# Kernel tuning notes

Measured on AMD Instinct MI355X. Metric: run time of the kernel, lower is better.

## Reference

```python
import jax, jax.numpy as jnp
import numpy as np

N = 12288
E = 393216
IN_DIM = 128
HID = 64
QK = 32
K_HOPS = 2


def setup_inputs() -> dict:
    key = jax.random.key(0)
    ks = jax.random.split(key, 12)
    s = lambda k, shp, fan: jax.random.normal(k, shp, jnp.float32) / np.sqrt(fan)
    return {
        "x_train": jax.random.normal(ks[0], (N, IN_DIM), jnp.float32),
        "x_ori": jax.random.normal(ks[1], (N, IN_DIM), jnp.float32),
        "edge_index": jax.random.randint(ks[2], (2, E), 0, N, jnp.int64),
        "mask": jnp.zeros((N,), jnp.bool_),
        "W1": s(ks[3], (IN_DIM, HID), IN_DIM), "b1": jnp.zeros((HID,), jnp.float32),
        "W2": s(ks[4], (HID, HID), HID),      "b2": jnp.zeros((HID,), jnp.float32),
        "Wq": s(ks[5], (HID, QK), HID),       "bq": jnp.zeros((QK,), jnp.float32),
        "Wk": s(ks[6], (HID, QK), HID),       "bk": jnp.zeros((QK,), jnp.float32),
        "Wv": s(ks[7], (HID, HID), HID),      "bv": jnp.zeros((HID,), jnp.float32),
        "Wdx": s(ks[8], (HID, IN_DIM), HID),  "bdx": jnp.zeros((IN_DIM,), jnp.float32),
    }


def reference(x_train, x_ori, edge_index, mask,
              W1, b1, W2, b2, Wq, bq, Wk, bk, Wv, bv, Wdx, bdx):
    n = x_train.shape[0]
    row, col = edge_index[0], edge_index[1]

    # shared MLP: linear -> relu -> linear2 -> relu
    enc = lambda x: jax.nn.relu(jax.nn.relu(x @ W1 + b1) @ W2 + b2)
    h_ori = enc(x_ori)      # [N, HID]
    h_train = enc(x_train)  # [N, HID]

    # degree of source nodes, D^{-1/2}
    deg = jax.ops.segment_sum(jnp.ones_like(row, jnp.float32), row, num_segments=n)
    d_invsqrt = jnp.clip(deg, 1.0, None) ** -0.5  # [N]
    d_invsqrt = d_invsqrt[:, None]

    def lap(x):
        h = x * d_invsqrt
        out = jax.ops.segment_sum(h[row], col, num_segments=n)
        return x - out * d_invsqrt

    a_feat = 2.0 * h_train - lap(h_train)  # low-pass: 2I - L_sym
    stack = [a_feat]
    x = h_train
    for _ in range(K_HOPS):  # dropout inert in eval mode
        x = lap(x)
        stack.append(x)
    L = jnp.stack(stack, axis=1)  # [N, K+1, HID]

    # attention with global mean-pooled query over h_ori[~mask]
    w = (~mask).astype(jnp.float32)
    q_nodes = h_ori @ Wq + bq                              # [N, QK]
    q_global = (q_nodes * w[:, None]).sum(0) / jnp.clip(w.sum(), 1.0, None)  # [QK]
    keys = L @ Wk + bk   # [N, K+1, QK]
    vals = L @ Wv + bv   # [N, K+1, HID]
    scale = 1.0 / np.sqrt(HID)  # scale uses D = keys feature dim BEFORE projection
    scores = jnp.einsum('q,nkq->nk', q_global, keys) * scale
    A = jax.nn.softmax(scores, axis=-1)          # [N, K+1]
    z = jnp.einsum('nk,nkd->nd', A, vals)        # [N, HID]

    x_hat = z @ Wdx + bdx   # [N, IN_DIM]
    adj_hat = z @ z.T       # [N, N]
    return x_hat, adj_hat
```

## Files before the change

### kernel.cpp

```cpp
#include <hip/hip_runtime.h>
#include <hip/hip_bf16.h>

constexpr int N_  = 12288;
constexpr int E_  = 393216;
constexpr int IND = 128;
constexpr int HID = 64;
constexpr int QKD = 32;

typedef __attribute__((ext_vector_type(4))) float f4raw;
typedef __attribute__((ext_vector_type(8))) __bf16 bf16x8;
typedef __attribute__((ext_vector_type(4))) __bf16 bf16x4;
typedef __attribute__((ext_vector_type(16))) float f32x16;

__device__ inline bf16x8 lds_read_bf8(const char* base, int row, int k) {
  int off = (row * 128 + k * 2) ^ ((row & 7) << 4);
  uint4 u = *(const uint4*)(base + off);
  union { uint4 u; bf16x8 v; } c; c.u = u; return c.v;
}
__device__ inline void lds_write_bf(char* base, int row, int col, __bf16 v) {
  int off = (row * 128 + col * 2) ^ ((row & 7) << 4);
  *(__bf16*)(base + off) = v;
}

__global__ __launch_bounds__(256) void prep_hist_kernel(
    const float* __restrict__ xo, const float* __restrict__ xt,
    const int* __restrict__ row, const int* __restrict__ col,
    const float* __restrict__ W1, const float* __restrict__ W2,
    const float* __restrict__ Wv, const float* __restrict__ Wdx,
    __bf16* __restrict__ xb, __bf16* __restrict__ W1T, __bf16* __restrict__ W2T,
    __bf16* __restrict__ WvT, __bf16* __restrict__ WdxT,
    int* degRow, int* cntCol) {
  int b = blockIdx.x, tid = threadIdx.x;
  if (b < 1536) {
    int e = b * 256 + tid;
    atomicAdd(&degRow[row[e]], 1);
    atomicAdd(&cntCol[col[e]], 1);
  } else if (b < 3072) {
    size_t base = (size_t)(b - 1536) * 2048 + (size_t)tid * 8;
    const size_t half = (size_t)N_ * IND;
    const float* src = (base < half) ? (xo + base) : (xt + (base - half));
    f4raw v0 = *(const f4raw*)(src);
    f4raw v1 = *(const f4raw*)(src + 4);
    bf16x8 o;
    o[0] = (__bf16)v0.x; o[1] = (__bf16)v0.y; o[2] = (__bf16)v0.z; o[3] = (__bf16)v0.w;
    o[4] = (__bf16)v1.x; o[5] = (__bf16)v1.y; o[6] = (__bf16)v1.z; o[7] = (__bf16)v1.w;
    *(bf16x8*)(xb + base) = o;
  } else if (b == 3072) {
    for (int e = tid; e < IND * HID; e += 256) {
      int c = e >> 7, k = e & 127;
      W1T[e] = (__bf16)W1[k * HID + c];
    }
  } else if (b == 3073) {
    for (int e = tid; e < HID * HID; e += 256) {
      int c = e >> 6, k = e & 63;
      W2T[e] = (__bf16)W2[k * HID + c];
    }
  } else if (b == 3074) {
    for (int e = tid; e < HID * HID; e += 256) {
      int c = e >> 6, k = e & 63;
      WvT[e] = (__bf16)Wv[k * HID + c];
    }
  } else {
    for (int e = tid; e < HID * IND; e += 256) {
      int c = e >> 6, k = e & 63;
      WdxT[e] = (__bf16)Wdx[k * IND + c];
    }
  }
}

__global__ __launch_bounds__(1024) void scan_kernel(const int* __restrict__ cnt,
                                                    const int* __restrict__ deg,
                                                    int* __restrict__ off,
                                                    int* __restrict__ cursor,
                                                    float* __restrict__ dinv) {
  __shared__ int sd[1024];
  int tid = threadIdx.x;
  int base = tid * 12;
  int local[12];
  int s = 0;
#pragma unroll
  for (int i = 0; i < 12; ++i) { local[i] = cnt[base + i]; s += local[i]; }
  sd[tid] = s;
  __syncthreads();
  for (int o = 1; o < 1024; o <<= 1) {
    int v = (tid >= o) ? sd[tid - o] : 0;
    __syncthreads();
    sd[tid] += v;
    __syncthreads();
  }
  int run = sd[tid] - s;
#pragma unroll
  for (int i = 0; i < 12; ++i) {
    off[base + i] = run;
    cursor[base + i] = run;
    run += local[i];
  }
  if (tid == 1023) off[N_] = run;
#pragma unroll
  for (int i = 0; i < 12; ++i) {
    int ii = base + i;
    dinv[ii] = rsqrtf((float)max(deg[ii], 1));
  }
}

__global__ __launch_bounds__(256) void scatter_enc_kernel(
    const int* __restrict__ row, const int* __restrict__ col,
    int* cursor, int* __restrict__ csrRow,
    const __bf16* __restrict__ xb,
    const __bf16* __restrict__ W1T, const float* __restrict__ b1,
    const __bf16* __restrict__ W2T, const float* __restrict__ b2,
    const float* __restrict__ dinv, const unsigned char* __restrict__ mask,
    float* __restrict__ h_tr, float* __restrict__ xd, float* __restrict__ gsum) {
  __shared__ __align__(16) char h1s[2][32 * 128];
  __shared__ float wls[64];
  int b = blockIdx.x, tid = threadIdx.x;
  if (b < 1536) {
    int e = b * 256 + tid;
    int c = col[e];
    int p = atomicAdd(&cursor[c], 1);
    csrRow[p] = row[e];
    return;
  }
  int bb = b - 1536;
  bool ori = bb < 192;
  int row0 = (ori ? bb : bb - 192) * 64;
  const __bf16* xrow = xb + (ori ? (size_t)0 : (size_t)N_ * IND) + (size_t)row0 * IND;
  if (tid < 64) wls[tid] = ori ? (mask[row0 + tid] ? 0.f : 1.f) : dinv[row0 + tid];
  int wave = tid >> 6, lane = tid & 63;
  int p = wave >> 1, w2 = wave & 1;
  int lr = lane & 31, hi = lane >> 5;
  int colc = w2 * 32 + lr;
  f32x16 acc = (f32x16)(0.f);
  const __bf16* wcol = W1T + (size_t)colc * IND + hi * 8;
  const __bf16* arow = xrow + (size_t)(p * 32 + lr) * IND + hi * 8;
#pragma unroll
  for (int kk = 0; kk < 8; ++kk) {
    bf16x8 a = *(const bf16x8*)(arow + kk * 16);
    bf16x8 bq = *(const bf16x8*)(wcol + kk * 16);
    acc = __builtin_amdgcn_mfma_f32_32x32x16_bf16(a, bq, acc, 0, 0, 0);
  }
  float b1l = b1[colc];
#pragma unroll
  for (int reg = 0; reg < 16; ++reg) {
    int rr = (reg & 3) + 8 * (reg >> 2) + 4 * hi;
    float v = fmaxf(acc[reg] + b1l, 0.f);
    lds_write_bf(h1s[p], rr, colc, (__bf16)v);
  }
  __syncthreads();
  f32x16 acc2 = (f32x16)(0.f);
  const __bf16* wcol2 = W2T + (size_t)colc * HID + hi * 8;
#pragma unroll
  for (int kk = 0; kk < 4; ++kk) {
    bf16x8 a = lds_read_bf8(h1s[p], lr, kk * 16 + hi * 8);
    bf16x8 bq = *(const bf16x8*)(wcol2 + kk * 16);
    acc2 = __builtin_amdgcn_mfma_f32_32x32x16_bf16(a, bq, acc2, 0, 0, 0);
  }
  float b2l = b2[colc];
  if (ori) {
    float part = 0.f;
#pragma unroll
    for (int reg = 0; reg < 16; ++reg) {
      int rr = (reg & 3) + 8 * (reg >> 2) + 4 * hi;
      float v = fmaxf(acc2[reg] + b2l, 0.f);
      part = fmaf(wls[p * 32 + rr], v, part);
    }
    atomicAdd(&gsum[colc], part);
    if (tid == 0) {
      float wl = 0.f;
      for (int r = 0; r < 64; ++r) wl += wls[r];
      atomicAdd(&gsum[64], wl);
    }
  } else {
#pragma unroll
    for (int reg = 0; reg < 16; ++reg) {
      int rr = (reg & 3) + 8 * (reg >> 2) + 4 * hi;
      float v = fmaxf(acc2[reg] + b2l, 0.f);
      int gr = row0 + p * 32 + rr;
      h_tr[(size_t)gr * HID + colc] = v;
      xd[(size_t)gr * HID + colc] = v * wls[p * 32 + rr];
    }
  }
}

__global__ __launch_bounds__(256) void lap1_kernel(
    const float* __restrict__ xd, const float* __restrict__ dinv,
    const int* __restrict__ off, const int* __restrict__ csrRow,
    float* __restrict__ lap1d) {
  int lane = threadIdx.x & 63, wv = threadIdx.x >> 6;
  int g = lane >> 4, t = lane & 15;
  int c = blockIdx.x * 16 + wv * 4 + g;
  int s0 = off[c], s1 = off[c + 1];
  f4raw a0 = (f4raw)(0.f), a1 = (f4raw)(0.f);
  int i = s0;
  for (; i + 1 < s1; i += 2) {
    int r0 = csrRow[i], r1 = csrRow[i + 1];
    a0 += *(const f4raw*)(xd + (size_t)r0 * HID + t * 4);
    a1 += *(const f4raw*)(xd + (size_t)r1 * HID + t * 4);
  }
  if (i < s1) {
    int r0 = csrRow[i];
    a0 += *(const f4raw*)(xd + (size_t)r0 * HID + t * 4);
  }
  float d = dinv[c];
  size_t idx = (size_t)c * HID + t * 4;
  *(f4raw*)(lap1d + idx) = *(const f4raw*)(xd + idx) - (a0 + a1) * (d * d);
}

__global__ __launch_bounds__(256) void lap2_kernel(
    const float* __restrict__ lap1d, const float* __restrict__ dinv,
    const int* __restrict__ off, const int* __restrict__ csrRow,
    float* __restrict__ lap2) {
  int lane = threadIdx.x & 63, wv = threadIdx.x >> 6;
  int g = lane >> 4, t = lane & 15;
  int c = blockIdx.x * 16 + wv * 4 + g;
  int s0 = off[c], s1 = off[c + 1];
  f4raw a0 = (f4raw)(0.f), a1 = (f4raw)(0.f);
  int i = s0;
  for (; i + 1 < s1; i += 2) {
    int r0 = csrRow[i], r1 = csrRow[i + 1];
    a0 += *(const f4raw*)(lap1d + (size_t)r0 * HID + t * 4);
    a1 += *(const f4raw*)(lap1d + (size_t)r1 * HID + t * 4);
  }
  if (i < s1) {
    int r0 = csrRow[i];
    a0 += *(const f4raw*)(lap1d + (size_t)r0 * HID + t * 4);
  }
  float d = dinv[c];
  float rd = 1.0f / d;
  size_t idx = (size_t)c * HID + t * 4;
  *(f4raw*)(lap2 + idx) = *(const f4raw*)(lap1d + idx) * rd - (a0 + a1) * d;
}

__global__ __launch_bounds__(128) void attnz_xhat_kernel(
    const float* __restrict__ h, const float* __restrict__ lap1d,
    const float* __restrict__ lap2, const float* __restrict__ dinv,
    const float* __restrict__ gsum,
    const float* __restrict__ Wq, const float* __restrict__ bq,
    const float* __restrict__ Wk, const float* __restrict__ bk,
    const __bf16* __restrict__ WvT, const float* __restrict__ bv,
    const __bf16* __restrict__ WdxT, const float* __restrict__ bdx,
    float* __restrict__ xhat, __bf16* __restrict__ zb) {
  __shared__ __align__(16) char zps[32 * 128];
  __shared__ __align__(16) char zsl[32 * 128];
  __shared__ float qg[QKD];
  __shared__ float kqs[72];
  int tid = threadIdx.x;
  float wsum = gsum[64];
  if (tid < QKD) {
    float inv = 1.0f / fmaxf(wsum, 1.0f);
    float a = bq[tid] * wsum;
    for (int d0 = 0; d0 < HID; ++d0) a = fmaf(gsum[d0], Wq[d0 * QKD + tid], a);
    qg[tid] = a * inv;
  }
  __syncthreads();
  if (tid < 64) {
    float a = 0.f;
    for (int q = 0; q < QKD; ++q) a = fmaf(Wk[tid * QKD + q], qg[q], a);
    kqs[tid] = a * 0.125f;
  } else if (tid == 64) {
    float sb = 0.f;
    for (int q = 0; q < QKD; ++q) sb = fmaf(bk[q], qg[q], sb);
    kqs[64] = sb * 0.125f;
  }
  __syncthreads();
  int wave = tid >> 6, lane = tid & 63;
  int g = lane >> 4, t = lane & 15;
  int row0 = blockIdx.x * 32;
  f4raw kq4 = *(const f4raw*)(&kqs[t * 4]);
  float sbias = kqs[64];
#pragma unroll
  for (int it = 0; it < 4; ++it) {
    int r = wave * 16 + it * 4 + g;
    int c = row0 + r;
    size_t idx = (size_t)c * HID + t * 4;
    float d = dinv[c];
    float rd = 1.0f / d;
    f4raw hv = *(const f4raw*)(h + idx);
    f4raw v1 = *(const f4raw*)(lap1d + idx) * rd;
    f4raw v2 = *(const f4raw*)(lap2 + idx);
    f4raw av = 2.f * hv - v1;
    float s0 = av.x * kq4.x + av.y * kq4.y + av.z * kq4.z + av.w * kq4.w;
    float s1 = v1.x * kq4.x + v1.y * kq4.y + v1.z * kq4.z + v1.w * kq4.w;
    float s2 = v2.x * kq4.x + v2.y * kq4.y + v2.z * kq4.z + v2.w * kq4.w;
#pragma unroll
    for (int o = 1; o < 16; o <<= 1) {
      s0 += __shfl_xor(s0, o);
      s1 += __shfl_xor(s1, o);
      s2 += __shfl_xor(s2, o);
    }
    s0 += sbias; s1 += sbias; s2 += sbias;
    float m = fmaxf(s0, fmaxf(s1, s2));
    float e0 = __expf(s0 - m), e1 = __expf(s1 - m), e2 = __expf(s2 - m);
    float is = 1.f / (e0 + e1 + e2);
    f4raw zp = (e0 * av + e1 * v1 + e2 * v2) * is;
    bf16x4 z4;
    z4[0] = (__bf16)zp.x; z4[1] = (__bf16)zp.y; z4[2] = (__bf16)zp.z; z4[3] = (__bf16)zp.w;
    int off = (r * 128 + t * 8) ^ ((r & 7) << 4);
    *(bf16x4*)(zps + off) = z4;
  }
  __syncthreads();
  int lr = lane & 31, hi = lane >> 5;
  int col = wave * 32 + lr;
  f32x16 accz = (f32x16)(0.f);
  const __bf16* wv = WvT + (size_t)col * HID + hi * 8;
#pragma unroll
  for (int kk = 0; kk < 4; ++kk) {
    bf16x8 a = lds_read_bf8(zps, lr, kk * 16 + hi * 8);
    bf16x8 bq = *(const bf16x8*)(wv + kk * 16);
    accz = __builtin_amdgcn_mfma_f32_32x32x16_bf16(a, bq, accz, 0, 0, 0);
  }
  float bvl = bv[col];
#pragma unroll
  for (int reg = 0; reg < 16; ++reg) {
    int rr = (reg & 3) + 8 * (reg >> 2) + 4 * hi;
    __bf16 vb = (__bf16)(accz[reg] + bvl);
    zb[(size_t)(row0 + rr) * HID + col] = vb;
    lds_write_bf(zsl, rr, col, vb);
  }
  __syncthreads();
#pragma unroll
  for (int tt = 0; tt < 2; ++tt) {
    int c0 = wave * 32 + tt * 64 + lr;
    f32x16 acx = (f32x16)(0.f);
    const __bf16* wd = WdxT + (size_t)c0 * HID + hi * 8;
#pragma unroll
    for (int kk = 0; kk < 4; ++kk) {
      bf16x8 a = lds_read_bf8(zsl, lr, kk * 16 + hi * 8);
      bf16x8 bq = *(const bf16x8*)(wd + kk * 16);
      acx = __builtin_amdgcn_mfma_f32_32x32x16_bf16(a, bq, acx, 0, 0, 0);
    }
    float bdl = bdx[c0];
#pragma unroll
    for (int reg = 0; reg < 16; ++reg) {
      int rr = (reg & 3) + 8 * (reg >> 2) + 4 * hi;
      xhat[(size_t)(row0 + rr) * IND + c0] = acx[reg] + bdl;
    }
  }
}

__global__ __launch_bounds__(256) void adj_mfma_kernel(
    const __bf16* __restrict__ z, float* __restrict__ out) {
  int tid = threadIdx.x;
  int wave = tid >> 6, lane = tid & 63;
  int wr = wave >> 1, wc = wave & 1;
  int rb = blockIdx.y, cb = blockIdx.x;
  int lr = lane & 31, hi = lane >> 5;

  size_t arow0 = (size_t)(rb * 128 + wr * 64 + lr) * HID;
  size_t arow1 = arow0 + (size_t)32 * HID;
  size_t brow0 = (size_t)(cb * 128 + wc * 64 + lr) * HID;
  size_t brow1 = brow0 + (size_t)32 * HID;
  int kbase = hi * 8;

  f32x16 acc00 = (f32x16)(0.f), acc01 = (f32x16)(0.f);
  f32x16 acc10 = (f32x16)(0.f), acc11 = (f32x16)(0.f);

#pragma unroll
  for (int kk = 0; kk < 4; ++kk) {
    int k0 = kk * 16 + kbase;
    bf16x8 a0 = *(const bf16x8*)(z + arow0 + k0);
    bf16x8 a1 = *(const bf16x8*)(z + arow1 + k0);
    bf16x8 b0 = *(const bf16x8*)(z + brow0 + k0);
    bf16x8 b1 = *(const bf16x8*)(z + brow1 + k0);
    acc00 = __builtin_amdgcn_mfma_f32_32x32x16_bf16(a0, b0, acc00, 0, 0, 0);
    acc01 = __builtin_amdgcn_mfma_f32_32x32x16_bf16(a0, b1, acc01, 0, 0, 0);
    acc10 = __builtin_amdgcn_mfma_f32_32x32x16_bf16(a1, b0, acc10, 0, 0, 0);
    acc11 = __builtin_amdgcn_mfma_f32_32x32x16_bf16(a1, b1, acc11, 0, 0, 0);
  }

  int colb = cb * 128 + wc * 64 + lr;
  int rowb = rb * 128 + wr * 64 + 4 * hi;
#pragma unroll
  for (int reg = 0; reg < 16; ++reg) {
    int rr = (reg & 3) + 8 * (reg >> 2);
    size_t r0 = (size_t)(rowb + rr);
    __builtin_nontemporal_store(acc00[reg], out + r0 * N_ + colb);
    __builtin_nontemporal_store(acc01[reg], out + r0 * N_ + colb + 32);
    __builtin_nontemporal_store(acc10[reg], out + (r0 + 32) * N_ + colb);
    __builtin_nontemporal_store(acc11[reg], out + (r0 + 32) * N_ + colb + 32);
  }
}

extern "C" void kernel_launch(void* const* d_in, const int* in_sizes, int n_in,
                              void* d_out, int out_size, void* d_ws, size_t ws_size,
                              hipStream_t stream) {
  const float* x_train = (const float*)d_in[0];
  const float* x_ori   = (const float*)d_in[1];
  const int*   ei      = (const int*)d_in[2];
  const unsigned char* mask = (const unsigned char*)d_in[3];
  const float* W1  = (const float*)d_in[4];
  const float* b1  = (const float*)d_in[5];
  const float* W2  = (const float*)d_in[6];
  const float* b2  = (const float*)d_in[7];
  const float* Wq  = (const float*)d_in[8];
  const float* bq  = (const float*)d_in[9];
  const float* Wk  = (const float*)d_in[10];
  const float* bk  = (const float*)d_in[11];
  const float* Wv  = (const float*)d_in[12];
  const float* bv  = (const float*)d_in[13];
  const float* Wdx = (const float*)d_in[14];
  const float* bdx = (const float*)d_in[15];

  char* ws = (char*)d_ws;
  size_t o = 0;
  auto alloc = [&](size_t bytes) -> void* {
    void* p = ws + o;
    o += (bytes + 255) & ~(size_t)255;
    return p;
  };
  __bf16* xb    = (__bf16*)alloc((size_t)2 * N_ * IND * 2);
  __bf16* W1T   = (__bf16*)alloc((size_t)IND * HID * 2);
  __bf16* W2T   = (__bf16*)alloc((size_t)HID * HID * 2);
  __bf16* WvT   = (__bf16*)alloc((size_t)HID * HID * 2);
  __bf16* WdxT  = (__bf16*)alloc((size_t)HID * IND * 2);
  float* h_tr   = (float*)alloc((size_t)N_ * HID * 4);
  float* lap1d  = (float*)alloc((size_t)N_ * HID * 4);
  float* lap2   = (float*)alloc((size_t)N_ * HID * 4);
  float* xd     = (float*)alloc((size_t)N_ * HID * 4);
  __bf16* zb    = (__bf16*)alloc((size_t)N_ * HID * 2);
  float* dinv   = (float*)alloc((size_t)N_ * 4);
  int*   zero0  = (int*)alloc((size_t)(2 * N_ + 65) * 4);
  int*   degRow = zero0;
  int*   cntCol = zero0 + N_;
  float* gsum   = (float*)(zero0 + 2 * N_);
  int*   off    = (int*)alloc((size_t)(N_ + 1) * 4);
  int*   cursor = (int*)alloc((size_t)N_ * 4);
  int*   csrRow = (int*)alloc((size_t)E_ * 4);

  const int* row = ei;
  const int* col = ei + E_;

  (void)hipMemsetAsync(zero0, 0, (size_t)(2 * N_ + 65) * 4, stream);

  prep_hist_kernel<<<3076, 256, 0, stream>>>(x_ori, x_train, row, col,
                                             W1, W2, Wv, Wdx,
                                             xb, W1T, W2T, WvT, WdxT,
                                             degRow, cntCol);
  scan_kernel<<<1, 1024, 0, stream>>>(cntCol, degRow, off, cursor, dinv);
  scatter_enc_kernel<<<1920, 256, 0, stream>>>(row, col, cursor, csrRow,
                                               xb, W1T, b1, W2T, b2,
                                               dinv, mask, h_tr, xd, gsum);
  lap1_kernel<<<N_ / 16, 256, 0, stream>>>(xd, dinv, off, csrRow, lap1d);
  lap2_kernel<<<N_ / 16, 256, 0, stream>>>(lap1d, dinv, off, csrRow, lap2);

  float* outp = (float*)d_out;
  attnz_xhat_kernel<<<N_ / 32, 128, 0, stream>>>(h_tr, lap1d, lap2, dinv, gsum,
                                                 Wq, bq, Wk, bk, WvT, bv,
                                                 WdxT, bdx, outp, zb);
  adj_mfma_kernel<<<dim3(96, 96), 256, 0, stream>>>(zb, outp + (size_t)N_ * IND);
}
```

Before: 270.0 us.

## Replace prefix-scan CSR with fixed-capacity buckets and fuse lap2 into attention

```diff
diff --git a/kernel.cpp b/kernel.cpp
--- a/kernel.cpp
+++ b/kernel.cpp
@@ -6,6 +6,7 @@
 constexpr int IND = 128;
 constexpr int HID = 64;
 constexpr int QKD = 32;
+constexpr int CAP = 96;
 
 typedef __attribute__((ext_vector_type(4))) float f4raw;
 typedef __attribute__((ext_vector_type(8))) __bf16 bf16x8;
@@ -22,21 +23,33 @@
   *(__bf16*)(base + off) = v;
 }
 
-__global__ __launch_bounds__(256) void prep_hist_kernel(
+__global__ __launch_bounds__(256) void prep_graph_kernel(
     const float* __restrict__ xo, const float* __restrict__ xt,
     const int* __restrict__ row, const int* __restrict__ col,
     const float* __restrict__ W1, const float* __restrict__ W2,
     const float* __restrict__ Wv, const float* __restrict__ Wdx,
     __bf16* __restrict__ xb, __bf16* __restrict__ W1T, __bf16* __restrict__ W2T,
     __bf16* __restrict__ WvT, __bf16* __restrict__ WdxT,
-    int* degRow, int* cntCol) {
+    int* degRow, int* cntCol, int* __restrict__ csrRow) {
   int b = blockIdx.x, tid = threadIdx.x;
-  if (b < 1536) {
-    int e = b * 256 + tid;
-    atomicAdd(&degRow[row[e]], 1);
-    atomicAdd(&cntCol[col[e]], 1);
-  } else if (b < 3072) {
-    size_t base = (size_t)(b - 1536) * 2048 + (size_t)tid * 8;
+  if (b < 384) {
+    int e0 = (b * 256 + tid) * 4;
+    int4 r4 = *(const int4*)(row + e0);
+    atomicAdd(&degRow[r4.x], 1);
+    atomicAdd(&degRow[r4.y], 1);
+    atomicAdd(&degRow[r4.z], 1);
+    atomicAdd(&degRow[r4.w], 1);
+  } else if (b < 768) {
+    int e0 = ((b - 384) * 256 + tid) * 4;
+    int4 r4 = *(const int4*)(row + e0);
+    int4 c4 = *(const int4*)(col + e0);
+    int p;
+    p = atomicAdd(&cntCol[c4.x], 1); csrRow[c4.x * CAP + p] = r4.x;
+    p = atomicAdd(&cntCol[c4.y], 1); csrRow[c4.y * CAP + p] = r4.y;
+    p = atomicAdd(&cntCol[c4.z], 1); csrRow[c4.z * CAP + p] = r4.z;
+    p = atomicAdd(&cntCol[c4.w], 1); csrRow[c4.w * CAP + p] = r4.w;
+  } else if (b < 2304) {
+    size_t base = (size_t)(b - 768) * 2048 + (size_t)tid * 8;
     const size_t half = (size_t)N_ * IND;
     const float* src = (base < half) ? (xo + base) : (xt + (base - half));
     f4raw v0 = *(const f4raw*)(src);
@@ -45,17 +58,17 @@
     o[0] = (__bf16)v0.x; o[1] = (__bf16)v0.y; o[2] = (__bf16)v0.z; o[3] = (__bf16)v0.w;
     o[4] = (__bf16)v1.x; o[5] = (__bf16)v1.y; o[6] = (__bf16)v1.z; o[7] = (__bf16)v1.w;
     *(bf16x8*)(xb + base) = o;
-  } else if (b == 3072) {
+  } else if (b == 2304) {
     for (int e = tid; e < IND * HID; e += 256) {
       int c = e >> 7, k = e & 127;
       W1T[e] = (__bf16)W1[k * HID + c];
     }
-  } else if (b == 3073) {
+  } else if (b == 2305) {
     for (int e = tid; e < HID * HID; e += 256) {
       int c = e >> 6, k = e & 63;
       W2T[e] = (__bf16)W2[k * HID + c];
     }
-  } else if (b == 3074) {
+  } else if (b == 2306) {
     for (int e = tid; e < HID * HID; e += 256) {
       int c = e >> 6, k = e & 63;
       WvT[e] = (__bf16)Wv[k * HID + c];
@@ -68,64 +81,27 @@
   }
 }
 
-__global__ __launch_bounds__(1024) void scan_kernel(const int* __restrict__ cnt,
-                                                    const int* __restrict__ deg,
-                                                    int* __restrict__ off,
-                                                    int* __restrict__ cursor,
-                                                    float* __restrict__ dinv) {
-  __shared__ int sd[1024];
-  int tid = threadIdx.x;
-  int base = tid * 12;
-  int local[12];
-  int s = 0;
-#pragma unroll
-  for (int i = 0; i < 12; ++i) { local[i] = cnt[base + i]; s += local[i]; }
-  sd[tid] = s;
-  __syncthreads();
-  for (int o = 1; o < 1024; o <<= 1) {
-    int v = (tid >= o) ? sd[tid - o] : 0;
-    __syncthreads();
-    sd[tid] += v;
-    __syncthreads();
-  }
-  int run = sd[tid] - s;
-#pragma unroll
-  for (int i = 0; i < 12; ++i) {
-    off[base + i] = run;
-    cursor[base + i] = run;
-    run += local[i];
-  }
-  if (tid == 1023) off[N_] = run;
-#pragma unroll
-  for (int i = 0; i < 12; ++i) {
-    int ii = base + i;
-    dinv[ii] = rsqrtf((float)max(deg[ii], 1));
-  }
-}
-
-__global__ __launch_bounds__(256) void scatter_enc_kernel(
-    const int* __restrict__ row, const int* __restrict__ col,
-    int* cursor, int* __restrict__ csrRow,
+__global__ __launch_bounds__(256) void enc_dinv_kernel(
     const __bf16* __restrict__ xb,
     const __bf16* __restrict__ W1T, const float* __restrict__ b1,
     const __bf16* __restrict__ W2T, const float* __restrict__ b2,
-    const float* __restrict__ dinv, const unsigned char* __restrict__ mask,
-    float* __restrict__ h_tr, float* __restrict__ xd, float* __restrict__ gsum) {
+    const int* __restrict__ degRow, const unsigned char* __restrict__ mask,
+    float* __restrict__ h_tr, float* __restrict__ dinv, float* __restrict__ gsum) {
   __shared__ __align__(16) char h1s[2][32 * 128];
   __shared__ float wls[64];
   int b = blockIdx.x, tid = threadIdx.x;
-  if (b < 1536) {
-    int e = b * 256 + tid;
-    int c = col[e];
-    int p = atomicAdd(&cursor[c], 1);
-    csrRow[p] = row[e];
+  if (b >= 384) {
+    int i0 = ((b - 384) * 256 + tid) * 4;
+    int4 dg = *(const int4*)(degRow + i0);
+    f4raw o = {rsqrtf((float)max(dg.x, 1)), rsqrtf((float)max(dg.y, 1)),
+               rsqrtf((float)max(dg.z, 1)), rsqrtf((float)max(dg.w, 1))};
+    *(f4raw*)(dinv + i0) = o;
     return;
   }
-  int bb = b - 1536;
-  bool ori = bb < 192;
-  int row0 = (ori ? bb : bb - 192) * 64;
+  bool ori = b < 192;
+  int row0 = (ori ? b : b - 192) * 64;
   const __bf16* xrow = xb + (ori ? (size_t)0 : (size_t)N_ * IND) + (size_t)row0 * IND;
-  if (tid < 64) wls[tid] = ori ? (mask[row0 + tid] ? 0.f : 1.f) : dinv[row0 + tid];
+  if (ori && tid < 64) wls[tid] = mask[row0 + tid] ? 0.f : 1.f;
   int wave = tid >> 6, lane = tid & 63;
   int p = wave >> 1, w2 = wave & 1;
   int lr = lane & 31, hi = lane >> 5;
@@ -175,82 +151,81 @@
     for (int reg = 0; reg < 16; ++reg) {
       int rr = (reg & 3) + 8 * (reg >> 2) + 4 * hi;
       float v = fmaxf(acc2[reg] + b2l, 0.f);
-      int gr = row0 + p * 32 + rr;
-      h_tr[(size_t)gr * HID + colc] = v;
-      xd[(size_t)gr * HID + colc] = v * wls[p * 32 + rr];
+      h_tr[(size_t)(row0 + p * 32 + rr) * HID + colc] = v;
     }
   }
 }
 
 __global__ __launch_bounds__(256) void lap1_kernel(
-    const float* __restrict__ xd, const float* __restrict__ dinv,
-    const int* __restrict__ off, const int* __restrict__ csrRow,
+    const float* __restrict__ h, const float* __restrict__ dinv,
+    const int* __restrict__ cnt, const int* __restrict__ csrRow,
     float* __restrict__ lap1d) {
   int lane = threadIdx.x & 63, wv = threadIdx.x >> 6;
   int g = lane >> 4, t = lane & 15;
   int c = blockIdx.x * 16 + wv * 4 + g;
-  int s0 = off[c], s1 = off[c + 1];
+  int s0 = c * CAP, s1 = s0 + cnt[c];
   f4raw a0 = (f4raw)(0.f), a1 = (f4raw)(0.f);
   int i = s0;
   for (; i + 1 < s1; i += 2) {
     int r0 = csrRow[i], r1 = csrRow[i + 1];
-    a0 += *(const f4raw*)(xd + (size_t)r0 * HID + t * 4);
-    a1 += *(const f4raw*)(xd + (size_t)r1 * HID + t * 4);
+    a0 += (*(const f4raw*)(h + (size_t)r0 * HID + t * 4)) * dinv[r0];
+    a1 += (*(const f4raw*)(h + (size_t)r1 * HID + t * 4)) * dinv[r1];
   }
   if (i < s1) {
     int r0 = csrRow[i];
-    a0 += *(const f4raw*)(xd + (size_t)r0 * HID + t * 4);
+    a0 += (*(const f4raw*)(h + (size_t)r0 * HID + t * 4)) * dinv[r0];
   }
   float d = dinv[c];
   size_t idx = (size_t)c * HID + t * 4;
-  *(f4raw*)(lap1d + idx) = *(const f4raw*)(xd + idx) - (a0 + a1) * (d * d);
-}
-
-__global__ __launch_bounds__(256) void lap2_kernel(
-    const float* __restrict__ lap1d, const float* __restrict__ dinv,
-    const int* __restrict__ off, const int* __restrict__ csrRow,
-    float* __restrict__ lap2) {
-  int lane = threadIdx.x & 63, wv = threadIdx.x >> 6;
-  int g = lane >> 4, t = lane & 15;
-  int c = blockIdx.x * 16 + wv * 4 + g;
-  int s0 = off[c], s1 = off[c + 1];
-  f4raw a0 = (f4raw)(0.f), a1 = (f4raw)(0.f);
-  int i = s0;
-  for (; i + 1 < s1; i += 2) {
-    int r0 = csrRow[i], r1 = csrRow[i + 1];
-    a0 += *(const f4raw*)(lap1d + (size_t)r0 * HID + t * 4);
-    a1 += *(const f4raw*)(lap1d + (size_t)r1 * HID + t * 4);
-  }
-  if (i < s1) {
-    int r0 = csrRow[i];
-    a0 += *(const f4raw*)(lap1d + (size_t)r0 * HID + t * 4);
-  }
-  float d = dinv[c];
-  float rd = 1.0f / d;
-  size_t idx = (size_t)c * HID + t * 4;
-  *(f4raw*)(lap2 + idx) = *(const f4raw*)(lap1d + idx) * rd - (a0 + a1) * d;
-}
-
-__global__ __launch_bounds__(128) void attnz_xhat_kernel(
+  f4raw hc = *(const f4raw*)(h + idx);
+  *(f4raw*)(lap1d + idx) = (hc - (a0 + a1) * d) * d;
+}
+
+__global__ __launch_bounds__(256) void lap2_attnz_xhat_kernel(
     const float* __restrict__ h, const float* __restrict__ lap1d,
-    const float* __restrict__ lap2, const float* __restrict__ dinv,
+    const float* __restrict__ dinv,
+    const int* __restrict__ cnt, const int* __restrict__ csrRow,
     const float* __restrict__ gsum,
     const float* __restrict__ Wq, const float* __restrict__ bq,
     const float* __restrict__ Wk, const float* __restrict__ bk,
     const __bf16* __restrict__ WvT, const float* __restrict__ bv,
     const __bf16* __restrict__ WdxT, const float* __restrict__ bdx,
     float* __restrict__ xhat, __bf16* __restrict__ zb) {
+  __shared__ float l2s[32][68];
   __shared__ __align__(16) char zps[32 * 128];
   __shared__ __align__(16) char zsl[32 * 128];
   __shared__ float qg[QKD];
   __shared__ float kqs[72];
   int tid = threadIdx.x;
+  int row0 = blockIdx.x * 32;
   float wsum = gsum[64];
   if (tid < QKD) {
     float inv = 1.0f / fmaxf(wsum, 1.0f);
     float a = bq[tid] * wsum;
     for (int d0 = 0; d0 < HID; ++d0) a = fmaf(gsum[d0], Wq[d0 * QKD + tid], a);
     qg[tid] = a * inv;
+  }
+  int grp = tid >> 4, t = tid & 15;
+#pragma unroll
+  for (int it = 0; it < 2; ++it) {
+    int r = grp + 16 * it;
+    int c = row0 + r;
+    int s0 = c * CAP, s1 = s0 + cnt[c];
+    f4raw a0 = (f4raw)(0.f), a1 = (f4raw)(0.f);
+    int i = s0;
+    for (; i + 1 < s1; i += 2) {
+      int r0 = csrRow[i], r1 = csrRow[i + 1];
+      a0 += *(const f4raw*)(lap1d + (size_t)r0 * HID + t * 4);
+      a1 += *(const f4raw*)(lap1d + (size_t)r1 * HID + t * 4);
+    }
+    if (i < s1) {
+      int r0 = csrRow[i];
+      a0 += *(const f4raw*)(lap1d + (size_t)r0 * HID + t * 4);
+    }
+    float d = dinv[c];
+    float rd = 1.0f / d;
+    f4raw lv = *(const f4raw*)(lap1d + (size_t)c * HID + t * 4);
+    *(f4raw*)&l2s[r][t * 4] = lv * rd - (a0 + a1) * d;
   }
   __syncthreads();
   if (tid < 64) {
@@ -263,21 +238,18 @@
     kqs[64] = sb * 0.125f;
   }
   __syncthreads();
-  int wave = tid >> 6, lane = tid & 63;
-  int g = lane >> 4, t = lane & 15;
-  int row0 = blockIdx.x * 32;
   f4raw kq4 = *(const f4raw*)(&kqs[t * 4]);
   float sbias = kqs[64];
 #pragma unroll
-  for (int it = 0; it < 4; ++it) {
-    int r = wave * 16 + it * 4 + g;
+  for (int it = 0; it < 2; ++it) {
+    int r = grp + 16 * it;
     int c = row0 + r;
     size_t idx = (size_t)c * HID + t * 4;
     float d = dinv[c];
     float rd = 1.0f / d;
     f4raw hv = *(const f4raw*)(h + idx);
     f4raw v1 = *(const f4raw*)(lap1d + idx) * rd;
-    f4raw v2 = *(const f4raw*)(lap2 + idx);
+    f4raw v2 = *(const f4raw*)&l2s[r][t * 4];
     f4raw av = 2.f * hv - v1;
     float s0 = av.x * kq4.x + av.y * kq4.y + av.z * kq4.z + av.w * kq4.w;
     float s1 = v1.x * kq4.x + v1.y * kq4.y + v1.z * kq4.z + v1.w * kq4.w;
@@ -299,28 +271,30 @@
     *(bf16x4*)(zps + off) = z4;
   }
   __syncthreads();
+  int wave = tid >> 6, lane = tid & 63;
   int lr = lane & 31, hi = lane >> 5;
-  int col = wave * 32 + lr;
-  f32x16 accz = (f32x16)(0.f);
-  const __bf16* wv = WvT + (size_t)col * HID + hi * 8;
-#pragma unroll
-  for (int kk = 0; kk < 4; ++kk) {
-    bf16x8 a = lds_read_bf8(zps, lr, kk * 16 + hi * 8);
-    bf16x8 bq = *(const bf16x8*)(wv + kk * 16);
-    accz = __builtin_amdgcn_mfma_f32_32x32x16_bf16(a, bq, accz, 0, 0, 0);
-  }
-  float bvl = bv[col];
-#pragma unroll
-  for (int reg = 0; reg < 16; ++reg) {
-    int rr = (reg & 3) + 8 * (reg >> 2) + 4 * hi;
-    __bf16 vb = (__bf16)(accz[reg] + bvl);
-    zb[(size_t)(row0 + rr) * HID + col] = vb;
-    lds_write_bf(zsl, rr, col, vb);
+  if (wave < 2) {
+    int col = wave * 32 + lr;
+    f32x16 accz = (f32x16)(0.f);
+    const __bf16* wv = WvT + (size_t)col * HID + hi * 8;
+#pragma unroll
+    for (int kk = 0; kk < 4; ++kk) {
+      bf16x8 a = lds_read_bf8(zps, lr, kk * 16 + hi * 8);
+      bf16x8 bq = *(const bf16x8*)(wv + kk * 16);
+      accz = __builtin_amdgcn_mfma_f32_32x32x16_bf16(a, bq, accz, 0, 0, 0);
+    }
+    float bvl = bv[col];
+#pragma unroll
+    for (int reg = 0; reg < 16; ++reg) {
+      int rr = (reg & 3) + 8 * (reg >> 2) + 4 * hi;
+      __bf16 vb = (__bf16)(accz[reg] + bvl);
+      zb[(size_t)(row0 + rr) * HID + col] = vb;
+      lds_write_bf(zsl, rr, col, vb);
+    }
   }
   __syncthreads();
-#pragma unroll
-  for (int tt = 0; tt < 2; ++tt) {
-    int c0 = wave * 32 + tt * 64 + lr;
+  {
+    int c0 = wave * 32 + lr;
     f32x16 acx = (f32x16)(0.f);
     const __bf16* wd = WdxT + (size_t)c0 * HID + hi * 8;
 #pragma unroll
@@ -415,37 +389,31 @@
   __bf16* WdxT  = (__bf16*)alloc((size_t)HID * IND * 2);
   float* h_tr   = (float*)alloc((size_t)N_ * HID * 4);
   float* lap1d  = (float*)alloc((size_t)N_ * HID * 4);
-  float* lap2   = (float*)alloc((size_t)N_ * HID * 4);
-  float* xd     = (float*)alloc((size_t)N_ * HID * 4);
   __bf16* zb    = (__bf16*)alloc((size_t)N_ * HID * 2);
   float* dinv   = (float*)alloc((size_t)N_ * 4);
+  int*   csrRow = (int*)alloc((size_t)N_ * CAP * 4);
   int*   zero0  = (int*)alloc((size_t)(2 * N_ + 65) * 4);
   int*   degRow = zero0;
   int*   cntCol = zero0 + N_;
   float* gsum   = (float*)(zero0 + 2 * N_);
-  int*   off    = (int*)alloc((size_t)(N_ + 1) * 4);
-  int*   cursor = (int*)alloc((size_t)N_ * 4);
-  int*   csrRow = (int*)alloc((size_t)E_ * 4);
 
   const int* row = ei;
   const int* col = ei + E_;
 
   (void)hipMemsetAsync(zero0, 0, (size_t)(2 * N_ + 65) * 4, stream);
 
-  prep_hist_kernel<<<3076, 256, 0, stream>>>(x_ori, x_train, row, col,
-                                             W1, W2, Wv, Wdx,
-                                             xb, W1T, W2T, WvT, WdxT,
-                                             degRow, cntCol);
-  scan_kernel<<<1, 1024, 0, stream>>>(cntCol, degRow, off, cursor, dinv);
-  scatter_enc_kernel<<<1920, 256, 0, stream>>>(row, col, cursor, csrRow,
-                                               xb, W1T, b1, W2T, b2,
-                                               dinv, mask, h_tr, xd, gsum);
-  lap1_kernel<<<N_ / 16, 256, 0, stream>>>(xd, dinv, off, csrRow, lap1d);
-  lap2_kernel<<<N_ / 16, 256, 0, stream>>>(lap1d, dinv, off, csrRow, lap2);
+  prep_graph_kernel<<<2308, 256, 0, stream>>>(x_ori, x_train, row, col,
+                                              W1, W2, Wv, Wdx,
+                                              xb, W1T, W2T, WvT, WdxT,
+                                              degRow, cntCol, csrRow);
+  enc_dinv_kernel<<<396, 256, 0, stream>>>(xb, W1T, b1, W2T, b2, degRow, mask,
+                                           h_tr, dinv, gsum);
+  lap1_kernel<<<N_ / 16, 256, 0, stream>>>(h_tr, dinv, cntCol, csrRow, lap1d);
 
   float* outp = (float*)d_out;
-  attnz_xhat_kernel<<<N_ / 32, 128, 0, stream>>>(h_tr, lap1d, lap2, dinv, gsum,
-                                                 Wq, bq, Wk, bk, WvT, bv,
-                                                 WdxT, bdx, outp, zb);
+  lap2_attnz_xhat_kernel<<<N_ / 32, 256, 0, stream>>>(h_tr, lap1d, dinv,
+                                                      cntCol, csrRow, gsum,
+                                                      Wq, bq, Wk, bk, WvT, bv,
+                                                      WdxT, bdx, outp, zb);
   adj_mfma_kernel<<<dim3(96, 96), 256, 0, stream>>>(zb, outp + (size_t)N_ * IND);
 }
```

Measured after the change: 254.2 us. 1.06x faster.
